# Kernel optimization log

Measured on AMD Instinct MI355X. Metric: run time of the kernel, lower is better.

Reference implementation:

```python
import jax, jax.numpy as jnp
import numpy as np

HID = 1024
DEPTH = 2

def _rhn_layer(x, Win, bin_, Wh, bh, Wt, bt):
    # x: [B, T, in]; returns outputs [B, T, H]
    B = x.shape[0]
    h0 = jnp.zeros((B, HID), dtype=x.dtype)
    xt = jnp.swapaxes(x, 0, 1)  # [T, B, in]

    def step(h_prev, x_t):
        h = x_t @ Win + bin_
        for i in range(DEPTH):
            t_gate = jax.nn.sigmoid(h @ Wt[i] + bt[i])
            h_layer = jnp.tanh(h @ Wh[i] + bh[i])
            h = t_gate * h_layer + (1.0 - t_gate) * h
        h_new = h + h_prev
        return h_new, h_new

    _, outs = jax.lax.scan(step, h0, xt)  # [T, B, H]
    return jnp.swapaxes(outs, 0, 1)


def setup_inputs() -> dict:
    key = jax.random.key(0)
    ks = jax.random.split(key, 16)
    B, T, IN, H, OUT = 64, 256, 128, HID, 128
    s = lambda fan_in: 1.0 / np.sqrt(fan_in)
    d = {}
    d["x"] = jax.random.normal(ks[0], (B, T, IN), dtype=jnp.float32)
    # layer 0 (input_size=IN)
    d["l0_Win"] = jax.random.uniform(ks[1], (IN, H), minval=-s(IN), maxval=s(IN))
    d["l0_bin"] = jax.random.uniform(ks[2], (H,), minval=-s(IN), maxval=s(IN))
    d["l0_Wh"] = jax.random.uniform(ks[3], (DEPTH, H, H), minval=-s(H), maxval=s(H))
    d["l0_bh"] = jax.random.uniform(ks[4], (DEPTH, H), minval=-s(H), maxval=s(H))
    d["l0_Wt"] = jax.random.uniform(ks[5], (DEPTH, H, H), minval=-s(H), maxval=s(H))
    d["l0_bt"] = jax.random.uniform(ks[6], (DEPTH, H), minval=-s(H), maxval=s(H))
    # layer 1 (input_size=H)
    d["l1_Win"] = jax.random.uniform(ks[7], (H, H), minval=-s(H), maxval=s(H))
    d["l1_bin"] = jax.random.uniform(ks[8], (H,), minval=-s(H), maxval=s(H))
    d["l1_Wh"] = jax.random.uniform(ks[9], (DEPTH, H, H), minval=-s(H), maxval=s(H))
    d["l1_bh"] = jax.random.uniform(ks[10], (DEPTH, H), minval=-s(H), maxval=s(H))
    d["l1_Wt"] = jax.random.uniform(ks[11], (DEPTH, H, H), minval=-s(H), maxval=s(H))
    d["l1_bt"] = jax.random.uniform(ks[12], (DEPTH, H), minval=-s(H), maxval=s(H))
    # final fc
    d["fc_W"] = jax.random.uniform(ks[13], (H, OUT), minval=-s(H), maxval=s(H))
    d["fc_b"] = jax.random.uniform(ks[14], (OUT,), minval=-s(H), maxval=s(H))
    return d


def reference(x, l0_Win, l0_bin, l0_Wh, l0_bh, l0_Wt, l0_bt,
              l1_Win, l1_bin, l1_Wh, l1_bh, l1_Wt, l1_bt, fc_W, fc_b):
    out = _rhn_layer(x, l0_Win, l0_bin, l0_Wh, l0_bh, l0_Wt, l0_bt)
    out = _rhn_layer(out, l1_Win, l1_bin, l1_Wh, l1_bh, l1_Wt, l1_bt)
    # forecast_horizon = 1 -> last time step only
    out = out[:, -1:, :] @ fc_W + fc_b  # [B, 1, OUT]
    return out
```

## Files before the change

kernel.cpp:

```cpp
#include <hip/hip_runtime.h>

typedef unsigned short u16;
typedef unsigned int u32;
typedef __bf16 bf16x8 __attribute__((ext_vector_type(8)));
typedef float floatx4 __attribute__((ext_vector_type(4)));

#define HID 1024
#define BATCH 64
#define SEQ 256
#define INDIM 128
#define OUTDIM 128
#define MROWS (BATCH*SEQ)

__device__ __forceinline__ float b2f(u16 u) {
    union { u32 u; float f; } v; v.u = ((u32)u) << 16; return v.f;
}
__device__ __forceinline__ u16 f2b(float f) {
    union { float f; u32 u; } v; v.f = f;
    u32 x = v.u;
    x += 0x7fffu + ((x >> 16) & 1u);
    return (u16)(x >> 16);
}
__device__ __forceinline__ float sigm(float x) { return 1.f / (1.f + __expf(-x)); }
__device__ __forceinline__ float tanh_f(float x) { return 2.f / (1.f + __expf(-2.f * x)) - 1.f; }

__device__ __forceinline__ void gld16(const u16* g, u16* l) {
    __builtin_amdgcn_global_load_lds(
        (const __attribute__((address_space(1))) void*)g,
        (__attribute__((address_space(3))) void*)l, 16, 0, 0);
}

__device__ __forceinline__ void bar_sync() {
    asm volatile("" ::: "memory");
    __builtin_amdgcn_s_barrier();
    asm volatile("" ::: "memory");
}
template <int N>
__device__ __forceinline__ void vm_bar() {
    asm volatile("s_waitcnt vmcnt(%0)" :: "n"(N) : "memory");
    __builtin_amdgcn_s_barrier();
    asm volatile("" ::: "memory");
}

__global__ void detect_dtype(const u16* __restrict__ w, int* __restrict__ flag) {
    __shared__ int s;
    if (threadIdx.x == 0) s = 0;
    __syncthreads();
    int bad = 0;
    for (int i = threadIdx.x; i < 4096; i += 256) {
        int e = (w[i] >> 7) & 0xff;
        if (e >= 127) bad = 1;
    }
    if (bad) atomicOr(&s, 1);
    __syncthreads();
    if (threadIdx.x == 0) *flag = s;
}

__device__ __forceinline__ int is_fp32(const u16* probe) {
    const int lane = threadIdx.x & 63;
    const int e = (probe[lane * 7] >> 7) & 0xff;
    return __ballot(e >= 127) != 0ULL;
}

struct CvtList { const void* s[7]; u16* d[7]; int n[7]; };

__global__ void convert7(CvtList C, const int* __restrict__ flag) {
    const int fp32 = *flag;
    const int z = blockIdx.y;
    const int n = C.n[z];
    const int stride = gridDim.x * 256;
    for (int i = blockIdx.x * 256 + threadIdx.x; i < n; i += stride) {
        u16 o;
        if (fp32) o = f2b(((const float*)C.s[z])[i]);
        else      o = ((const u16*)C.s[z])[i];
        C.d[z][i] = o;
    }
}

struct TListO {
    const void* s[10];
    u16*        d[10];
    int         R[10];
    int         Cc[10];
    long        off[10];
};

__global__ void transpose10(TListO L, const int* __restrict__ flag) {
    const int fp32 = *flag;
    const int z = blockIdx.z;
    const void* src = L.s[z];
    u16*        dst = L.d[z];
    const int R  = L.R[z];
    const int Cc = L.Cc[z];
    const long zo = L.off[z];
    const int tr = blockIdx.y * 32, tc = blockIdx.x * 32;
    if (tr >= R || tc >= Cc) return;
    __align__(16) __shared__ u16 t[32][33];
    const int tx = threadIdx.x, ty = threadIdx.y;
#pragma unroll
    for (int i = 0; i < 4; ++i) {
        const int r = ty + i * 8;
        const long e = zo + (long)(tr + r) * Cc + tc + tx;
        u16 v;
        if (fp32) v = f2b(((const float*)src)[e]);
        else      v = ((const u16*)src)[e];
        t[r][tx] = v;
    }
    __syncthreads();
#pragma unroll
    for (int i = 0; i < 4; ++i) {
        const int r = ty + i * 8;
        dst[(size_t)(tc + r) * R + tr + tx] = t[tx][r];
    }
}

__device__ __forceinline__ void tile_swizzle(int& m0, int& n0) {
    const int lin = blockIdx.y * gridDim.x + blockIdx.x;
    const int xcd = lin & 7;
    const int loc = lin >> 3;
    m0 = (xcd * 16 + (loc & 15)) * 128;
    n0 = (loc >> 4) * 128;
}

__device__ __forceinline__ void tile_swizzle8(int& m0, int& n0) {
    const int lin = blockIdx.x;
    const int xcd = lin & 7;
    const int loc = lin >> 3;
    m0 = (xcd * 8 + (loc & 7)) * 256;
    n0 = (loc >> 3) * 128;
}

__global__ __launch_bounds__(256, 2) void gemm128(
    const u16* __restrict__ A, const u16* __restrict__ BT,
    const u16* __restrict__ bias, u16* __restrict__ C,
    int M, int N, int K)
{
    __align__(16) __shared__ u16 As[128 * 64];
    __align__(16) __shared__ u16 Bs[128 * 64];

    const int tid  = threadIdx.x;
    const int lane = tid & 63;
    const int wid  = tid >> 6;
    const int wr   = wid >> 1;
    const int wc   = wid & 1;

    int m0, n0;
    tile_swizzle(m0, n0);

    floatx4 acc[4][4] = {};

    const int srow = lane >> 3;
    const int scol = 8 * ((lane & 7) ^ (lane >> 3));
    const int cb   = wid * 4;
    const u16* Ag[4]; const u16* Bg[4];
    u16 *Al[4], *Bl[4];
#pragma unroll
    for (int j = 0; j < 4; ++j) {
        const int c = cb + j;
        const int r = c * 8 + srow;
        Ag[j] = A  + (size_t)(m0 + r) * K + scol;
        Bg[j] = BT + (size_t)(n0 + r) * K + scol;
        Al[j] = As + c * 512;
        Bl[j] = Bs + c * 512;
    }

    const int quad = lane >> 4;
    const int l16  = lane & 15;
    const int swz  = l16 & 7;

    const int nk = K >> 6;
    for (int kt = 0; kt < nk; ++kt) {
        __syncthreads();
#pragma unroll
        for (int j = 0; j < 4; ++j) {
            gld16(Ag[j], Al[j]);  gld16(Bg[j], Bl[j]);
            Ag[j] += 64; Bg[j] += 64;
        }
        __syncthreads();

#pragma unroll
        for (int kk = 0; kk < 2; ++kk) {
            const int slot = ((kk * 4 + quad) ^ swz) * 8;
            bf16x8 af[4], bfr[4];
#pragma unroll
            for (int i = 0; i < 4; ++i) {
                af[i]  = *(const bf16x8*)(As + (wr * 64 + i * 16 + l16) * 64 + slot);
                bfr[i] = *(const bf16x8*)(Bs + (wc * 64 + i * 16 + l16) * 64 + slot);
            }
#pragma unroll
            for (int i = 0; i < 4; ++i)
#pragma unroll
                for (int j = 0; j < 4; ++j)
                    acc[i][j] = __builtin_amdgcn_mfma_f32_16x16x32_bf16(af[i], bfr[j], acc[i][j], 0, 0, 0);
        }
    }

#pragma unroll
    for (int i = 0; i < 4; ++i) {
        const int rowb = m0 + wr * 64 + i * 16 + quad * 4;
#pragma unroll
        for (int j = 0; j < 4; ++j) {
            const int col = n0 + wc * 64 + j * 16 + l16;
            const float bv = b2f(bias[col]);
#pragma unroll
            for (int r = 0; r < 4; ++r)
                C[(size_t)(rowb + r) * N + col] = f2b(acc[i][j][r] + bv);
        }
    }
}

__device__ __forceinline__ void hw8_mainloop(
    const u16* __restrict__ A, const u16* __restrict__ WtT, const u16* __restrict__ WhT,
    int m0, int n0, int K,
    floatx4 (&acct)[4][4], floatx4 (&acch)[4][4])
{
    __align__(16) __shared__ u16 lds[65536];

    const int tid  = threadIdx.x;
    const int lane = tid & 63;
    const int wid  = tid >> 6;
    const int wr   = wid >> 1;
    const int wc   = wid & 1;

    const int srow = lane >> 3;
    const int scol = 8 * ((lane & 7) ^ srow);

    const u16* Ag = A   + (size_t)(m0 + wid * 32 + srow) * K + scol;
    const u16* Tg = WtT + (size_t)(n0 + wid * 16 + srow) * K + scol;
    const u16* Hg = WhT + (size_t)(n0 + wid * 16 + srow) * K + scol;
    const size_t K8 = (size_t)K * 8;

    u16* dA = lds + wid * 2048;
    u16* dT = lds + 16384 + wid * 1024;
    u16* dH = lds + 24576 + wid * 1024;

    const int quad = lane >> 4;
    const int l16  = lane & 15;
    const int swz  = l16 & 7;
    const int s0 = (quad ^ swz) * 8;
    const int s1 = ((4 + quad) ^ swz) * 8;
    const int ra = wr * 64 + l16;
    const int rb = wc * 64 + l16;

    gld16(Ag,           dA);
    gld16(Ag +     K8,  dA + 512);
    gld16(Ag + 2 * K8,  dA + 1024);
    gld16(Ag + 3 * K8,  dA + 1536);
    gld16(Tg,           dT);
    gld16(Tg +     K8,  dT + 512);
    gld16(Hg,           dH);
    gld16(Hg +     K8,  dH + 512);
    Ag += 64; Tg += 64; Hg += 64;

    const int nk = K >> 6;
    for (int kt = 0; kt < nk; ++kt) {
        const int  cur = kt & 1;
        const int  nb  = (cur ^ 1) * 32768;
        const bool pf  = (kt + 1 < nk);
        const u16* Sa = lds + cur * 32768;
        const u16* St = Sa + 16384;
        const u16* Sh = Sa + 24576;

        bf16x8 af[4], bq[4];

        vm_bar<2>();
        if (pf) { gld16(Ag, dA + nb); gld16(Ag + K8, dA + nb + 512); }
#pragma unroll
        for (int i = 0; i < 4; ++i) {
            af[i] = *(const bf16x8*)(Sa + (ra + i * 16) * 64 + s0);
            bq[i] = *(const bf16x8*)(St + (rb + i * 16) * 64 + s0);
        }
        __builtin_amdgcn_s_setprio(1);
#pragma unroll
        for (int i = 0; i < 4; ++i)
#pragma unroll
            for (int j = 0; j < 4; ++j)
                acct[i][j] = __builtin_amdgcn_mfma_f32_16x16x32_bf16(af[i], bq[j], acct[i][j], 0, 0, 0);
        __builtin_amdgcn_s_setprio(0);

        if (pf) { vm_bar<2>(); gld16(Ag + 2 * K8, dA + nb + 1024); gld16(Ag + 3 * K8, dA + nb + 1536); }
        else    { vm_bar<0>(); }
#pragma unroll
        for (int i = 0; i < 4; ++i)
            bq[i] = *(const bf16x8*)(Sh + (rb + i * 16) * 64 + s0);
        __builtin_amdgcn_s_setprio(1);
#pragma unroll
        for (int i = 0; i < 4; ++i)
#pragma unroll
            for (int j = 0; j < 4; ++j)
                acch[i][j] = __builtin_amdgcn_mfma_f32_16x16x32_bf16(af[i], bq[j], acch[i][j], 0, 0, 0);
        __builtin_amdgcn_s_setprio(0);

        bar_sync();
        if (pf) { gld16(Tg, dT + nb); gld16(Tg + K8, dT + nb + 512); }
#pragma unroll
        for (int i = 0; i < 4; ++i) {
            af[i] = *(const bf16x8*)(Sa + (ra + i * 16) * 64 + s1);
            bq[i] = *(const bf16x8*)(St + (rb + i * 16) * 64 + s1);
        }
        __builtin_amdgcn_s_setprio(1);
#pragma unroll
        for (int i = 0; i < 4; ++i)
#pragma unroll
            for (int j = 0; j < 4; ++j)
                acct[i][j] = __builtin_amdgcn_mfma_f32_16x16x32_bf16(af[i], bq[j], acct[i][j], 0, 0, 0);
        __builtin_amdgcn_s_setprio(0);

        bar_sync();
        if (pf) { gld16(Hg, dH + nb); gld16(Hg + K8, dH + nb + 512); }
#pragma unroll
        for (int i = 0; i < 4; ++i)
            bq[i] = *(const bf16x8*)(Sh + (rb + i * 16) * 64 + s1);
        __builtin_amdgcn_s_setprio(1);
#pragma unroll
        for (int i = 0; i < 4; ++i)
#pragma unroll
            for (int j = 0; j < 4; ++j)
                acch[i][j] = __builtin_amdgcn_mfma_f32_16x16x32_bf16(af[i], bq[j], acch[i][j], 0, 0, 0);
        __builtin_amdgcn_s_setprio(0);

        Ag += 64; Tg += 64; Hg += 64;
    }
}

__global__ __launch_bounds__(512, 2) void gemm_hw8(
    const u16* __restrict__ A,
    const u16* __restrict__ WtT,
    const u16* __restrict__ WhT,
    const u16* __restrict__ bt, const u16* __restrict__ bh,
    u16* __restrict__ Hout,
    int M, int N, int K)
{
    int m0, n0;
    tile_swizzle8(m0, n0);

    floatx4 acct[4][4] = {};
    floatx4 acch[4][4] = {};
    hw8_mainloop(A, WtT, WhT, m0, n0, K, acct, acch);

    const int tid  = threadIdx.x;
    const int lane = tid & 63;
    const int wid  = tid >> 6;
    const int wr   = wid >> 1;
    const int wc   = wid & 1;
    const int quad = lane >> 4;
    const int l16  = lane & 15;

#pragma unroll
    for (int i = 0; i < 4; ++i) {
        const int rowb = m0 + wr * 64 + i * 16 + quad * 4;
#pragma unroll
        for (int j = 0; j < 4; ++j) {
            const int col = n0 + wc * 64 + j * 16 + l16;
            const float btv = b2f(bt[col]);
            const float bhv = b2f(bh[col]);
#pragma unroll
            for (int r = 0; r < 4; ++r) {
                const size_t idx = (size_t)(rowb + r) * N + col;
                const float hold = b2f(A[idx]);
                const float tg = sigm(acct[i][j][r] + btv);
                const float hl = tanh_f(acch[i][j][r] + bhv);
                Hout[idx] = f2b(hold + tg * (hl - hold));
            }
        }
    }
}

__global__ __launch_bounds__(512, 2) void gemm_hw8_sum(
    const u16* __restrict__ A,
    const u16* __restrict__ WtT,
    const u16* __restrict__ WhT,
    const u16* __restrict__ bt, const u16* __restrict__ bh,
    float* __restrict__ hsum,
    int M, int N, int K)
{
    int m0, n0;
    tile_swizzle8(m0, n0);

    floatx4 acct[4][4] = {};
    floatx4 acch[4][4] = {};
    hw8_mainloop(A, WtT, WhT, m0, n0, K, acct, acch);

    const int tid  = threadIdx.x;
    const int lane = tid & 63;
    const int wid  = tid >> 6;
    const int wr   = wid >> 1;
    const int wc   = wid & 1;
    const int quad = lane >> 4;
    const int l16  = lane & 15;

    const int b = m0 >> 8;
#pragma unroll
    for (int j = 0; j < 4; ++j) {
        const int col = n0 + wc * 64 + j * 16 + l16;
        const float btv = b2f(bt[col]);
        const float bhv = b2f(bh[col]);
        float colsum = 0.f;
#pragma unroll
        for (int i = 0; i < 4; ++i) {
            const int rowb = m0 + wr * 64 + i * 16 + quad * 4;
#pragma unroll
            for (int r = 0; r < 4; ++r) {
                const size_t idx = (size_t)(rowb + r) * N + col;
                const float hold = b2f(A[idx]);
                const float tg = sigm(acct[i][j][r] + btv);
                const float hl = tanh_f(acch[i][j][r] + bhv);
                colsum += hold + tg * (hl - hold);
            }
        }
        colsum += __shfl_xor(colsum, 16, 64);
        colsum += __shfl_xor(colsum, 32, 64);
        if (quad == 0)
            atomicAdd(&hsum[(size_t)b * HID + col], colsum);
    }
}

__global__ void zero_hf(float* __restrict__ p) {
    p[blockIdx.x * 256 + threadIdx.x] = 0.f;
}

__global__ void cumsum_t(u16* g) {
    const int id = blockIdx.x * 256 + threadIdx.x;
    const int b = id >> 10, f = id & 1023;
    size_t base = (size_t)b * SEQ * HID + f;
    float acc = 0.f;
#pragma unroll 4
    for (int t = 0; t < SEQ; ++t) {
        size_t idx = base + (size_t)t * HID;
        acc += b2f(g[idx]);
        g[idx] = f2b(acc);
    }
}

__global__ void fc_final(const float* __restrict__ hf, const void* __restrict__ W,
                         const void* __restrict__ bias, void* __restrict__ out) {
    __shared__ float sh[HID];
    const int fp32 = is_fp32((const u16*)W);
    const int b = blockIdx.x, o = threadIdx.x;
    for (int k = o; k < HID; k += 128) sh[k] = hf[(size_t)b * HID + k];
    __syncthreads();
    float acc;
    if (fp32) {
        acc = ((const float*)bias)[o];
        for (int k = 0; k < HID; ++k)
            acc += sh[k] * ((const float*)W)[(size_t)k * OUTDIM + o];
        ((float*)out)[b * OUTDIM + o] = acc;
    } else {
        acc = b2f(((const u16*)bias)[o]);
        for (int k = 0; k < HID; ++k)
            acc += sh[k] * b2f(((const u16*)W)[(size_t)k * OUTDIM + o]);
        ((u16*)out)[b * OUTDIM + o] = f2b(acc);
    }
}

extern "C" void kernel_launch(void* const* d_in, const int* in_sizes, int n_in,
                              void* d_out, int out_size, void* d_ws, size_t ws_size,
                              hipStream_t stream) {
    const void* x      = d_in[0];
    const void* l0_Win = d_in[1];
    const void* l0_bin = d_in[2];
    const void* l0_Wh  = d_in[3];
    const void* l0_bh  = d_in[4];
    const void* l0_Wt  = d_in[5];
    const void* l0_bt  = d_in[6];
    const void* l1_Win = d_in[7];
    const void* l1_bin = d_in[8];
    const void* l1_Wh  = d_in[9];
    const void* l1_bh  = d_in[10];
    const void* l1_Wt  = d_in[11];
    const void* l1_bt  = d_in[12];
    const void* fc_W   = d_in[13];
    const void* fc_b   = d_in[14];

    char* ws = (char*)d_ws;
    u16* Pa = (u16*)(ws);
    u16* Pb = (u16*)(ws + 33554432);
    u16* xc = Pb;
    u16* tW = (u16*)(ws + 67108864);
    u16* tWin0 = tW;
    u16* tWt00 = tWin0 + 131072;
    u16* tWt01 = tWt00 + 1048576;
    u16* tWh00 = tWt01 + 1048576;
    u16* tWh01 = tWh00 + 1048576;
    u16* tWin1 = tWh01 + 1048576;
    u16* tWt10 = tWin1 + 1048576;
    u16* tWt11 = tWt10 + 1048576;
    u16* tWh10 = tWt11 + 1048576;
    u16* tWh11 = tWh10 + 1048576;
    u16* smallb = tWh11 + 1048576;
    u16* binc0 = smallb;
    u16* bhc0  = binc0 + 1024;
    u16* btc0  = bhc0 + 2048;
    u16* binc1 = btc0 + 2048;
    u16* bhc1  = binc1 + 1024;
    u16* btc1  = bhc1 + 2048;
    int* flag  = (int*)(btc1 + 2048);
    float* hfinal = (float*)Pb;

    detect_dtype<<<1, 256, 0, stream>>>((const u16*)l0_Wh, flag);

    const long DD = (long)HID * HID;
    TListO L;
    L.s[0] = l0_Win; L.d[0] = tWin0; L.R[0] = INDIM; L.Cc[0] = HID; L.off[0] = 0;
    L.s[1] = l0_Wt;  L.d[1] = tWt00; L.R[1] = HID;   L.Cc[1] = HID; L.off[1] = 0;
    L.s[2] = l0_Wt;  L.d[2] = tWt01; L.R[2] = HID;   L.Cc[2] = HID; L.off[2] = DD;
    L.s[3] = l0_Wh;  L.d[3] = tWh00; L.R[3] = HID;   L.Cc[3] = HID; L.off[3] = 0;
    L.s[4] = l0_Wh;  L.d[4] = tWh01; L.R[4] = HID;   L.Cc[4] = HID; L.off[4] = DD;
    L.s[5] = l1_Win; L.d[5] = tWin1; L.R[5] = HID;   L.Cc[5] = HID; L.off[5] = 0;
    L.s[6] = l1_Wt;  L.d[6] = tWt10; L.R[6] = HID;   L.Cc[6] = HID; L.off[6] = 0;
    L.s[7] = l1_Wt;  L.d[7] = tWt11; L.R[7] = HID;   L.Cc[7] = HID; L.off[7] = DD;
    L.s[8] = l1_Wh;  L.d[8] = tWh10; L.R[8] = HID;   L.Cc[8] = HID; L.off[8] = 0;
    L.s[9] = l1_Wh;  L.d[9] = tWh11; L.R[9] = HID;   L.Cc[9] = HID; L.off[9] = DD;
    transpose10<<<dim3(32, 32, 10), dim3(32, 8), 0, stream>>>(L, flag);

    CvtList C7;
    C7.s[0] = x;      C7.d[0] = xc;    C7.n[0] = MROWS * INDIM;
    C7.s[1] = l0_bin; C7.d[1] = binc0; C7.n[1] = HID;
    C7.s[2] = l0_bh;  C7.d[2] = bhc0;  C7.n[2] = 2 * HID;
    C7.s[3] = l0_bt;  C7.d[3] = btc0;  C7.n[3] = 2 * HID;
    C7.s[4] = l1_bin; C7.d[4] = binc1; C7.n[4] = HID;
    C7.s[5] = l1_bh;  C7.d[5] = bhc1;  C7.n[5] = 2 * HID;
    C7.s[6] = l1_bt;  C7.d[6] = btc1;  C7.n[6] = 2 * HID;
    convert7<<<dim3(512, 7), 256, 0, stream>>>(C7, flag);

    gemm128<<<dim3(8, 128), 256, 0, stream>>>(xc, tWin0, binc0, Pa, MROWS, HID, INDIM);
    gemm_hw8<<<512, 512, 0, stream>>>(Pa, tWt00, tWh00, btc0, bhc0, Pb, MROWS, HID, HID);
    gemm_hw8<<<512, 512, 0, stream>>>(Pb, tWt01, tWh01, btc0 + HID, bhc0 + HID, Pa, MROWS, HID, HID);
    cumsum_t<<<256, 256, 0, stream>>>(Pa);

    gemm128<<<dim3(8, 128), 256, 0, stream>>>(Pa, tWin1, binc1, Pb, MROWS, HID, HID);
    gemm_hw8<<<512, 512, 0, stream>>>(Pb, tWt10, tWh10, btc1, bhc1, Pa, MROWS, HID, HID);
    zero_hf<<<256, 256, 0, stream>>>(hfinal);
    gemm_hw8_sum<<<512, 512, 0, stream>>>(Pa, tWt11, tWh11, btc1 + HID, bhc1 + HID,
                                          hfinal, MROWS, HID, HID);

    fc_final<<<64, 128, 0, stream>>>(hfinal, fc_W, fc_b, d_out);
}
```

Baseline: 558.2 us.

## Reorder K-loop phases to finish T-gate before H and restructure prefetch barriers

Reorganizes the double-buffered K loop of the fused highway GEMM so both K-halves of the transform-gate MFMAs run before the H-path MFMAs. The A fragments for both halves are kept in registers (af0/af1), and the global-to-LDS prefetch issue points and vmcnt waits are regrouped around the new phase order. The aim is fewer LDS reloads of A and better overlap of prefetch with MFMA work. The cost is extra VGPR pressure from holding two A fragment sets, and barrier placement changes that could introduce LDS races if any wait count is wrong.

```diff
diff --git a/kernel.cpp b/kernel.cpp
--- a/kernel.cpp
+++ b/kernel.cpp
@@ -242,15 +242,16 @@
     const int ra = wr * 64 + l16;
     const int rb = wc * 64 + l16;
 
+    gld16(Tg,           dT);
+    gld16(Tg +     K8,  dT + 512);
     gld16(Ag,           dA);
     gld16(Ag +     K8,  dA + 512);
     gld16(Ag + 2 * K8,  dA + 1024);
     gld16(Ag + 3 * K8,  dA + 1536);
-    gld16(Tg,           dT);
-    gld16(Tg +     K8,  dT + 512);
     gld16(Hg,           dH);
     gld16(Hg +     K8,  dH + 512);
     Ag += 64; Tg += 64; Hg += 64;
+    vm_bar<2>();
 
     const int nk = K >> 6;
     for (int kt = 0; kt < nk; ++kt) {
@@ -261,62 +262,74 @@
         const u16* St = Sa + 16384;
         const u16* Sh = Sa + 24576;
 
-        bf16x8 af[4], bq[4];
-
-        vm_bar<2>();
-        if (pf) { gld16(Ag, dA + nb); gld16(Ag + K8, dA + nb + 512); }
+        bf16x8 af0[4], af1[4], bq[4];
+
 #pragma unroll
         for (int i = 0; i < 4; ++i) {
-            af[i] = *(const bf16x8*)(Sa + (ra + i * 16) * 64 + s0);
-            bq[i] = *(const bf16x8*)(St + (rb + i * 16) * 64 + s0);
-        }
+            af0[i] = *(const bf16x8*)(Sa + (ra + i * 16) * 64 + s0);
+            bq[i]  = *(const bf16x8*)(St + (rb + i * 16) * 64 + s0);
+        }
+        if (pf) {
+            gld16(Tg,      dT + nb);  gld16(Tg + K8, dT + nb + 512);
+            gld16(Ag,      dA + nb);  gld16(Ag + K8, dA + nb + 512);
+        }
+        bar_sync();
         __builtin_amdgcn_s_setprio(1);
 #pragma unroll
         for (int i = 0; i < 4; ++i)
 #pragma unroll
             for (int j = 0; j < 4; ++j)
-                acct[i][j] = __builtin_amdgcn_mfma_f32_16x16x32_bf16(af[i], bq[j], acct[i][j], 0, 0, 0);
+                acct[i][j] = __builtin_amdgcn_mfma_f32_16x16x32_bf16(af0[i], bq[j], acct[i][j], 0, 0, 0);
         __builtin_amdgcn_s_setprio(0);
 
-        if (pf) { vm_bar<2>(); gld16(Ag + 2 * K8, dA + nb + 1024); gld16(Ag + 3 * K8, dA + nb + 1536); }
-        else    { vm_bar<0>(); }
+#pragma unroll
+        for (int i = 0; i < 4; ++i) {
+            af1[i] = *(const bf16x8*)(Sa + (ra + i * 16) * 64 + s1);
+            bq[i]  = *(const bf16x8*)(St + (rb + i * 16) * 64 + s1);
+        }
+        if (pf) {
+            gld16(Ag + 2 * K8, dA + nb + 1024);
+            gld16(Ag + 3 * K8, dA + nb + 1536);
+            vm_bar<6>();
+        } else {
+            vm_bar<0>();
+        }
+        __builtin_amdgcn_s_setprio(1);
+#pragma unroll
+        for (int i = 0; i < 4; ++i)
+#pragma unroll
+            for (int j = 0; j < 4; ++j)
+                acct[i][j] = __builtin_amdgcn_mfma_f32_16x16x32_bf16(af1[i], bq[j], acct[i][j], 0, 0, 0);
+        __builtin_amdgcn_s_setprio(0);
+
 #pragma unroll
         for (int i = 0; i < 4; ++i)
             bq[i] = *(const bf16x8*)(Sh + (rb + i * 16) * 64 + s0);
+        bar_sync();
         __builtin_amdgcn_s_setprio(1);
 #pragma unroll
         for (int i = 0; i < 4; ++i)
 #pragma unroll
             for (int j = 0; j < 4; ++j)
-                acch[i][j] = __builtin_amdgcn_mfma_f32_16x16x32_bf16(af[i], bq[j], acch[i][j], 0, 0, 0);
+                acch[i][j] = __builtin_amdgcn_mfma_f32_16x16x32_bf16(af0[i], bq[j], acch[i][j], 0, 0, 0);
         __builtin_amdgcn_s_setprio(0);
 
-        bar_sync();
-        if (pf) { gld16(Tg, dT + nb); gld16(Tg + K8, dT + nb + 512); }
-#pragma unroll
-        for (int i = 0; i < 4; ++i) {
-            af[i] = *(const bf16x8*)(Sa + (ra + i * 16) * 64 + s1);
-            bq[i] = *(const bf16x8*)(St + (rb + i * 16) * 64 + s1);
-        }
-        __builtin_amdgcn_s_setprio(1);
-#pragma unroll
-        for (int i = 0; i < 4; ++i)
-#pragma unroll
-            for (int j = 0; j < 4; ++j)
-                acct[i][j] = __builtin_amdgcn_mfma_f32_16x16x32_bf16(af[i], bq[j], acct[i][j], 0, 0, 0);
-        __builtin_amdgcn_s_setprio(0);
-
-        bar_sync();
-        if (pf) { gld16(Hg, dH + nb); gld16(Hg + K8, dH + nb + 512); }
 #pragma unroll
         for (int i = 0; i < 4; ++i)
             bq[i] = *(const bf16x8*)(Sh + (rb + i * 16) * 64 + s1);
+        if (pf) {
+            gld16(Hg,      dH + nb);
+            gld16(Hg + K8, dH + nb + 512);
+            vm_bar<2>();
+        } else {
+            bar_sync();
+        }
         __builtin_amdgcn_s_setprio(1);
 #pragma unroll
         for (int i = 0; i < 4; ++i)
 #pragma unroll
             for (int j = 0; j < 4; ++j)
-                acch[i][j] = __builtin_amdgcn_mfma_f32_16x16x32_bf16(af[i], bq[j], acch[i][j], 0, 0, 0);
+                acch[i][j] = __builtin_amdgcn_mfma_f32_16x16x32_bf16(af1[i], bq[j], acch[i][j], 0, 0, 0);
         __builtin_amdgcn_s_setprio(0);
 
         Ag += 64; Tg += 64; Hg += 64;
```

New measurement: 538.0 us. 1.04x faster.
